# Kernel tuning notes

Hardware: AMD Instinct MI355X
Metric: run time of the kernel (lower is better)

The kernel has to match this reference:

```python
import jax, jax.numpy as jnp
import numpy as np
import math

B, S, D = 4, 2048, 1024

def setup_inputs() -> dict:
    key = jax.random.key(0)
    k1, k2, k3, k4 = jax.random.split(key, 4)
    scale = 1.0 / math.sqrt(D)
    return {
        "x": jax.random.normal(k1, (B, S, D), dtype=jnp.float32),
        "w_q": jax.random.normal(k2, (D, D), dtype=jnp.float32) * scale,
        "w_k": jax.random.normal(k3, (D, D), dtype=jnp.float32) * scale,
        "w_v": jax.random.normal(k4, (D, D), dtype=jnp.float32) * scale,
        "causal": 1,
    }

def reference(x, w_q, w_k, w_v, causal):
    # QKV projections: nn.Linear(dim, dim, bias=False) -> x @ W.T
    q = jnp.einsum('bsd,ed->bse', x, w_q)
    k = jnp.einsum('bsd,ed->bse', x, w_k)
    v = jnp.einsum('bsd,ed->bse', x, w_v)
    d_k = q.shape[-1]
    scores = jnp.einsum('bqd,bkd->bqk', q, k) / jnp.sqrt(jnp.asarray(d_k, q.dtype))
    if causal:
        seq_len = q.shape[-2]
        mask = jnp.triu(jnp.ones((seq_len, seq_len), dtype=bool), k=1)
        scores = jnp.where(mask, jnp.asarray(-jnp.inf, scores.dtype), scores)
    weights = jax.nn.softmax(scores, axis=-1)
    return jnp.einsum('bqk,bkd->bqd', weights, v)
```

## Files before the change

### kernel.cpp

```cpp
#include <hip/hip_runtime.h>
#include <stdint.h>

typedef unsigned short u16;
typedef __attribute__((ext_vector_type(8))) __bf16 bf16x8;
typedef __attribute__((ext_vector_type(4))) float f32x4;

__device__ __forceinline__ u16 f2bf(float f) {
  unsigned u = __float_as_uint(f);
  u += 0x7FFF + ((u >> 16) & 1);
  return (u16)(u >> 16);
}

__device__ __forceinline__ float bf2f(u16 h) {
  return __uint_as_float(((unsigned)h) << 16);
}

__device__ __forceinline__ void llds16(const u16* g, u16* l) {
  __builtin_amdgcn_global_load_lds(
      (const __attribute__((address_space(1))) void*)g,
      (__attribute__((address_space(3))) void*)l, 16, 0, 0);
}

__global__ __launch_bounds__(256) void cast_all(
    const float* __restrict__ x, const float* __restrict__ wq,
    const float* __restrict__ wk, const float* __restrict__ wv,
    u16* __restrict__ xb, u16* __restrict__ wb, float* __restrict__ lsum) {
  int i = blockIdx.x * 256 + threadIdx.x;
  if (i < 8192) lsum[i] = 0.f;
  const float* src; u16* dst; int off;
  if (i < 2097152)      { src = x;  dst = xb;            off = i; }
  else if (i < 2359296) { src = wq; dst = wb;            off = i - 2097152; }
  else if (i < 2621440) { src = wk; dst = wb + 1048576;  off = i - 2359296; }
  else                  { src = wv; dst = wb + 2097152;  off = i - 2621440; }
  float4 f = ((const float4*)src)[off];
  ushort4 o;
  o.x = f2bf(f.x); o.y = f2bf(f.y); o.z = f2bf(f.z); o.w = f2bf(f.w);
  ((ushort4*)dst)[off] = o;
}

template<int MODE>
__global__ __launch_bounds__(256) void gemm_nt(
    const u16* __restrict__ A, long long sA, int lda,
    const u16* __restrict__ B, long long sB, int ldb,
    void* __restrict__ Cp, long long sC, int ldc,
    int K, u16* __restrict__ vt, float scale,
    float* __restrict__ lsum, const int* __restrict__ causalp) {
  const int t = threadIdx.x;
  const int causal = (MODE == 0) ? 1 : causalp[0];

  int rt = blockIdx.x, ct = blockIdx.y;

  const int rowbase = rt * 128;
  const int colbase = ct * 128;
  const u16* Ab = A + (long long)blockIdx.z * sA;
  const u16* Bb = B + (long long)blockIdx.z * sB;

  int Keff = K;
  if (MODE == 2 && causal) Keff = min(K, rowbase + 128);

  __shared__ u16 As[8192];
  __shared__ u16 Bs[8192];

  const int lane = t & 63;
  const int wv = t >> 6;
  const int wr = wv >> 1;
  const int wc = wv & 1;
  const int quad = lane >> 4;
  const int lr = lane & 15;

  f32x4 acc[4][4];
  const f32x4 zero = {0.f, 0.f, 0.f, 0.f};
#pragma unroll
  for (int i = 0; i < 4; ++i)
#pragma unroll
    for (int j = 0; j < 4; ++j) acc[i][j] = zero;

  {
    const int csw = (t & 7) ^ ((t >> 3) & 7);
    const u16* ga = Ab + (long long)(rowbase + (t >> 3)) * lda + csw * 8;
    const u16* gb = Bb + (long long)(colbase + (t >> 3)) * ldb + csw * 8;
    const long long ra = 32LL * lda, rb = 32LL * ldb;
    u16* la = As + t * 8;
    u16* lb = Bs + t * 8;

    const int m7 = lr & 7;
    const int a_base = (wr * 64 + lr) * 64 + ((quad ^ m7) * 8);
    const int b_base = (wc * 64 + lr) * 64 + ((quad ^ m7) * 8);

    for (int k0 = 0; k0 < Keff; k0 += 64) {
      __syncthreads();
#pragma unroll
      for (int i = 0; i < 4; ++i) {
        llds16(ga + k0 + i * ra, la + i * 2048);
        llds16(gb + k0 + i * rb, lb + i * 2048);
      }
      __syncthreads();
#pragma unroll
      for (int ks = 0; ks < 2; ++ks) {
        const int ko = ks ? 32 : 0;
        bf16x8 af[4], bfv[4];
#pragma unroll
        for (int tm = 0; tm < 4; ++tm)
          af[tm] = *(const bf16x8*)(As + ((a_base + tm * 1024) ^ ko));
#pragma unroll
        for (int tn = 0; tn < 4; ++tn)
          bfv[tn] = *(const bf16x8*)(Bs + ((b_base + tn * 1024) ^ ko));
#pragma unroll
        for (int tm = 0; tm < 4; ++tm)
#pragma unroll
          for (int tn = 0; tn < 4; ++tn)
            acc[tm][tn] = __builtin_amdgcn_mfma_f32_16x16x32_bf16(
                af[tm], bfv[tn], acc[tm][tn], 0, 0, 0);
      }
    }
  }

  if (MODE == 0 && colbase >= 2048) {
#pragma unroll
    for (int tm = 0; tm < 4; ++tm) {
      int s0 = rowbase + wr * 64 + tm * 16 + quad * 4;
      int b = s0 >> 11;
      int sl = s0 & 2047;
#pragma unroll
      for (int tn = 0; tn < 4; ++tn) {
        int e = colbase - 2048 + wc * 64 + tn * 16 + lr;
        ushort4 o;
        o.x = f2bf(acc[tm][tn][0]);
        o.y = f2bf(acc[tm][tn][1]);
        o.z = f2bf(acc[tm][tn][2]);
        o.w = f2bf(acc[tm][tn][3]);
        *(ushort4*)(vt + ((long long)(b * 1024 + e)) * 2048 + sl) = o;
      }
    }
    return;
  }

#pragma unroll
  for (int tm = 0; tm < 4; ++tm) {
#pragma unroll
    for (int r = 0; r < 4; ++r) {
      const int grow = rowbase + wr * 64 + tm * 16 + quad * 4 + r;
      float li, rsum = 0.f;
      if (MODE == 2) li = __builtin_amdgcn_rcpf(lsum[blockIdx.z * 2048 + grow]);
#pragma unroll
      for (int tn = 0; tn < 4; ++tn) {
        const int gcol = colbase + wc * 64 + tn * 16 + lr;
        float val = acc[tm][tn][r];
        if (MODE == 0) {
          ((u16*)Cp)[(long long)grow * ldc + gcol] = f2bf(val);
        } else if (MODE == 1) {
          u16* C = (u16*)Cp + (long long)blockIdx.z * sC;
          float ex = (causal && gcol > grow) ? 0.f : __expf(val * scale);
          C[(long long)grow * ldc + gcol] = f2bf(ex);
          rsum += ex;
        } else {
          float* C = (float*)Cp + (long long)blockIdx.z * sC;
          C[(long long)grow * ldc + gcol] = val * li;
        }
      }
      if (MODE == 1) {
#pragma unroll
        for (int o = 8; o > 0; o >>= 1) rsum += __shfl_xor(rsum, o, 64);
        if (lr == 0)
          atomicAdd(&lsum[blockIdx.z * 2048 + grow], rsum);
      }
    }
  }
}

template<int MODE>
__device__ __forceinline__ void gemm_core(
    int rt, int ct, int zb, int causal, u16* As, u16* Bs,
    const u16* __restrict__ A, long long sA, int lda,
    const u16* __restrict__ B, long long sB, int ldb,
    void* __restrict__ Cp, long long sC, int ldc,
    int K, float scale, float* __restrict__ lsum) {
  const int t = threadIdx.x;

  const int rowbase = rt * 128;
  const int colbase = ct * 128;
  const u16* Ab = A + (long long)zb * sA;
  const u16* Bb = B + (long long)zb * sB;

  int Keff = K;
  if (MODE == 2 && causal) Keff = min(K, rowbase + 128);

  const int lane = t & 63;
  const int wv = t >> 6;
  const int wr = wv >> 1;
  const int wc = wv & 1;
  const int quad = lane >> 4;
  const int lr = lane & 15;

  f32x4 acc[4][4];
  const f32x4 zero = {0.f, 0.f, 0.f, 0.f};
#pragma unroll
  for (int i = 0; i < 4; ++i)
#pragma unroll
    for (int j = 0; j < 4; ++j) acc[i][j] = zero;

  {
    const int csw = (t & 7) ^ ((t >> 3) & 7);
    const u16* ga = Ab + (long long)(rowbase + (t >> 3)) * lda + csw * 8;
    const u16* gb = Bb + (long long)(colbase + (t >> 3)) * ldb + csw * 8;
    const long long ra = 32LL * lda, rb = 32LL * ldb;
    u16* la = As + t * 8;
    u16* lb = Bs + t * 8;

    const int m7 = lr & 7;
    const int a_base = (wr * 64 + lr) * 64 + ((quad ^ m7) * 8);
    const int b_base = (wc * 64 + lr) * 64 + ((quad ^ m7) * 8);

#pragma unroll
    for (int i = 0; i < 4; ++i) {
      llds16(ga + i * ra, la + i * 2048);
      llds16(gb + i * rb, lb + i * 2048);
    }
    __syncthreads();
    for (int k0 = 0; k0 < Keff; k0 += 64) {
      const int nb = ((k0 >> 6) & 1) ^ 1;
      const int bo = (nb ^ 1) << 13;
      if (k0 + 64 < Keff) {
#pragma unroll
        for (int i = 0; i < 4; ++i) {
          llds16(ga + (k0 + 64) + i * ra, la + nb * 8192 + i * 2048);
          llds16(gb + (k0 + 64) + i * rb, lb + nb * 8192 + i * 2048);
        }
      }
#pragma unroll
      for (int ks = 0; ks < 2; ++ks) {
        const int ko = ks ? 32 : 0;
        bf16x8 af[4], bfv[4];
#pragma unroll
        for (int tm = 0; tm < 4; ++tm)
          af[tm] = *(const bf16x8*)(As + bo + ((a_base + tm * 1024) ^ ko));
#pragma unroll
        for (int tn = 0; tn < 4; ++tn)
          bfv[tn] = *(const bf16x8*)(Bs + bo + ((b_base + tn * 1024) ^ ko));
#pragma unroll
        for (int tm = 0; tm < 4; ++tm)
#pragma unroll
          for (int tn = 0; tn < 4; ++tn)
            acc[tm][tn] = __builtin_amdgcn_mfma_f32_16x16x32_bf16(
                af[tm], bfv[tn], acc[tm][tn], 0, 0, 0);
      }
      __syncthreads();
    }
  }

#pragma unroll
  for (int tm = 0; tm < 4; ++tm) {
#pragma unroll
    for (int r = 0; r < 4; ++r) {
      const int grow = rowbase + wr * 64 + tm * 16 + quad * 4 + r;
      float li, rsum = 0.f;
      if (MODE == 2) li = __builtin_amdgcn_rcpf(lsum[zb * 2048 + grow]);
#pragma unroll
      for (int tn = 0; tn < 4; ++tn) {
        const int gcol = colbase + wc * 64 + tn * 16 + lr;
        float val = acc[tm][tn][r];
        if (MODE == 1) {
          u16* C = (u16*)Cp + (long long)zb * sC;
          float ex = (causal && gcol > grow) ? 0.f : __expf(val * scale);
          C[(long long)grow * ldc + gcol] = f2bf(ex);
          rsum += ex;
        } else {
          float* C = (float*)Cp + (long long)zb * sC;
          C[(long long)grow * ldc + gcol] = val * li;
        }
      }
      if (MODE == 1) {
#pragma unroll
        for (int o = 8; o > 0; o >>= 1) rsum += __shfl_xor(rsum, o, 64);
        if (lr == 0)
          atomicAdd(&lsum[zb * 2048 + grow], rsum);
      }
    }
  }
}

__global__ __launch_bounds__(256) void gemm_sc(
    const u16* __restrict__ qk, u16* __restrict__ sb,
    float* __restrict__ lsum, const int* __restrict__ causalp) {
  __shared__ u16 As[16384];
  __shared__ u16 Bs[16384];
  const int causal = causalp[0];
  const int zb = blockIdx.z;
  const int xcd = blockIdx.x & 7;
  const int chunk = ((blockIdx.x >> 3) + 8 * blockIdx.z) & 31;
  int rt, ct;
  if (chunk < 17) {
    int i2 = xcd * 17 + chunk, c = 0;
    while (i2 >= 16 - c) { i2 -= 16 - c; ++c; }
    ct = c; rt = c + i2;
  } else {
    if (causal) return;
    int i2 = xcd * 15 + (chunk - 17), r = 0;
    while (i2 >= r + 1) { i2 -= r + 1; ++r; }
    rt = i2; ct = r + 1;
  }
  gemm_core<1>(rt, ct, zb, causal, As, Bs,
               qk, 2048LL * 2048, 2048, qk + 1024, 2048LL * 2048, 2048,
               sb, 2048LL * 2048, 2048, 1024, 0.03125f, lsum);
}

__global__ __launch_bounds__(256) void gemm_pv(
    const u16* __restrict__ sb, const u16* __restrict__ vtb,
    float* __restrict__ out, float* __restrict__ lsum,
    const int* __restrict__ causalp) {
  __shared__ u16 As[16384];
  __shared__ u16 Bs[16384];
  const int causal = causalp[0];
  const int s = ((blockIdx.x & 7) << 6) + (blockIdx.x >> 3);
  const int zb = s >> 7;
  const int ct = (s & 127) >> 4;
  const int m = s & 15;
  const int rt = (s & 32) ? m : 15 - m;
  gemm_core<2>(rt, ct, zb, causal, As, Bs,
               sb, 2048LL * 2048, 2048, vtb, 1024LL * 2048, 2048,
               out, 2048LL * 1024, 1024, 2048, 1.0f, lsum);
}

extern "C" void kernel_launch(void* const* d_in, const int* in_sizes, int n_in,
                              void* d_out, int out_size, void* d_ws, size_t ws_size,
                              hipStream_t stream) {
  const float* x  = (const float*)d_in[0];
  const float* wq = (const float*)d_in[1];
  const float* wk = (const float*)d_in[2];
  const float* wv = (const float*)d_in[3];
  const int* causal = (const int*)d_in[4];
  float* out = (float*)d_out;

  char* ws = (char*)d_ws;
  u16* xb = (u16*)(ws);
  u16* wb = (u16*)(ws + 16777216);
  u16* qk = (u16*)(ws + 23068672);
  u16* vt = (u16*)(ws + 56623104);
  u16* sb = (u16*)(ws + 73400320);
  float* lsum = (float*)(ws + 106954752);

  cast_all<<<11264, 256, 0, stream>>>(x, wq, wk, wv, xb, wb, lsum);

  gemm_nt<0><<<dim3(64, 24, 1), 256, 0, stream>>>(
      xb, 0, 1024, wb, 0, 1024, qk, 0, 2048, 1024, vt, 1.0f, nullptr, causal);

  gemm_sc<<<dim3(256, 1, 4), 256, 0, stream>>>(qk, sb, lsum, causal);

  gemm_pv<<<dim3(512, 1, 1), 256, 0, stream>>>(sb, vt, out, lsum, causal);
}
```

Baseline: 231.3 us.

## Replace 128x128 four-wave attention GEMMs with single-wave 64x64 tile kernels

The score and PV GEMMs move from 256-thread blocks computing 128x128 tiles with double-buffered LDS to 64-thread single-wave blocks computing 64x64 tiles with one LDS buffer. The aim is finer causal skipping, since only lower-triangle 64x64 tiles run and the PV K range is trimmed per 64 rows, plus more blocks to fill the CUs. In exchange, each tile reuses its loaded data less, global-to-LDS prefetch overlap is gone because every K step syncs around a fresh load, and the XCD-aware block ordering is dropped.

```diff
diff --git a/kernel.cpp b/kernel.cpp
--- a/kernel.cpp
+++ b/kernel.cpp
@@ -169,74 +169,81 @@
 }
 
 template<int MODE>
-__device__ __forceinline__ void gemm_core(
-    int rt, int ct, int zb, int causal, u16* As, u16* Bs,
+__global__ __launch_bounds__(64) void tile64(
     const u16* __restrict__ A, long long sA, int lda,
     const u16* __restrict__ B, long long sB, int ldb,
     void* __restrict__ Cp, long long sC, int ldc,
-    int K, float scale, float* __restrict__ lsum) {
+    int K, float scale, float* __restrict__ lsum,
+    const int* __restrict__ causalp) {
   const int t = threadIdx.x;
-
-  const int rowbase = rt * 128;
-  const int colbase = ct * 128;
+  const int causal = causalp[0];
+
+  int rt, ct, zb;
+  if (MODE == 1) {
+    const int j = blockIdx.x;
+    zb = j >> 10;
+    const int rem = j & 1023;
+    rt = rem >> 5;
+    ct = rem & 31;
+    if (causal && ct > rt) return;
+  } else {
+    const int j = blockIdx.x;
+    zb = j >> 9;
+    const int rem = j & 511;
+    rt = 31 - (rem >> 4);
+    ct = rem & 15;
+  }
+
+  const int rowbase = rt * 64;
+  const int colbase = ct * 64;
   const u16* Ab = A + (long long)zb * sA;
   const u16* Bb = B + (long long)zb * sB;
 
   int Keff = K;
-  if (MODE == 2 && causal) Keff = min(K, rowbase + 128);
-
-  const int lane = t & 63;
-  const int wv = t >> 6;
-  const int wr = wv >> 1;
-  const int wc = wv & 1;
-  const int quad = lane >> 4;
-  const int lr = lane & 15;
+  if (MODE == 2 && causal) Keff = min(K, rowbase + 64);
+
+  __shared__ u16 As[4096];
+  __shared__ u16 Bs[4096];
+
+  const int quad = t >> 4;
+  const int lr = t & 15;
 
   f32x4 acc[4][4];
   const f32x4 zero = {0.f, 0.f, 0.f, 0.f};
 #pragma unroll
   for (int i = 0; i < 4; ++i)
 #pragma unroll
-    for (int j = 0; j < 4; ++j) acc[i][j] = zero;
+    for (int j2 = 0; j2 < 4; ++j2) acc[i][j2] = zero;
 
   {
     const int csw = (t & 7) ^ ((t >> 3) & 7);
     const u16* ga = Ab + (long long)(rowbase + (t >> 3)) * lda + csw * 8;
     const u16* gb = Bb + (long long)(colbase + (t >> 3)) * ldb + csw * 8;
-    const long long ra = 32LL * lda, rb = 32LL * ldb;
+    const long long ra = 8LL * lda, rb = 8LL * ldb;
     u16* la = As + t * 8;
     u16* lb = Bs + t * 8;
 
     const int m7 = lr & 7;
-    const int a_base = (wr * 64 + lr) * 64 + ((quad ^ m7) * 8);
-    const int b_base = (wc * 64 + lr) * 64 + ((quad ^ m7) * 8);
-
-#pragma unroll
-    for (int i = 0; i < 4; ++i) {
-      llds16(ga + i * ra, la + i * 2048);
-      llds16(gb + i * rb, lb + i * 2048);
-    }
-    __syncthreads();
+    const int fbase = lr * 64 + ((quad ^ m7) * 8);
+
     for (int k0 = 0; k0 < Keff; k0 += 64) {
-      const int nb = ((k0 >> 6) & 1) ^ 1;
-      const int bo = (nb ^ 1) << 13;
-      if (k0 + 64 < Keff) {
-#pragma unroll
-        for (int i = 0; i < 4; ++i) {
-          llds16(ga + (k0 + 64) + i * ra, la + nb * 8192 + i * 2048);
-          llds16(gb + (k0 + 64) + i * rb, lb + nb * 8192 + i * 2048);
-        }
-      }
+      __syncthreads();
+#pragma unroll
+      for (int i = 0; i < 8; ++i) {
+        llds16(ga + k0 + i * ra, la + i * 512);
+        llds16(gb + k0 + i * rb, lb + i * 512);
+      }
+      __syncthreads();
 #pragma unroll
       for (int ks = 0; ks < 2; ++ks) {
         const int ko = ks ? 32 : 0;
         bf16x8 af[4], bfv[4];
 #pragma unroll
         for (int tm = 0; tm < 4; ++tm)
-          af[tm] = *(const bf16x8*)(As + bo + ((a_base + tm * 1024) ^ ko));
+          af[tm] = *(const bf16x8*)(As + ((fbase + tm * 1024) ^ ko));
 #pragma unroll
         for (int tn = 0; tn < 4; ++tn)
-          bfv[tn] = *(const bf16x8*)(Bs + bo + ((b_base + tn * 1024) ^ ko));
+          bfv[tn] = *(const bf16x8*)(Bs + ((fbase + tn * 1024) ^ ko));
 #pragma unroll
         for (int tm = 0; tm < 4; ++tm)
 #pragma unroll
@@ -244,7 +251,6 @@
             acc[tm][tn] = __builtin_amdgcn_mfma_f32_16x16x32_bf16(
                 af[tm], bfv[tn], acc[tm][tn], 0, 0, 0);
       }
-      __syncthreads();
     }
   }
 
@@ -252,12 +258,12 @@
   for (int tm = 0; tm < 4; ++tm) {
 #pragma unroll
     for (int r = 0; r < 4; ++r) {
-      const int grow = rowbase + wr * 64 + tm * 16 + quad * 4 + r;
+      const int grow = rowbase + tm * 16 + quad * 4 + r;
       float li, rsum = 0.f;
       if (MODE == 2) li = __builtin_amdgcn_rcpf(lsum[zb * 2048 + grow]);
 #pragma unroll
       for (int tn = 0; tn < 4; ++tn) {
-        const int gcol = colbase + wc * 64 + tn * 16 + lr;
+        const int gcol = colbase + tn * 16 + lr;
         float val = acc[tm][tn][r];
         if (MODE == 1) {
           u16* C = (u16*)Cp + (long long)zb * sC;
@@ -279,48 +285,6 @@
   }
 }
 
-__global__ __launch_bounds__(256) void gemm_sc(
-    const u16* __restrict__ qk, u16* __restrict__ sb,
-    float* __restrict__ lsum, const int* __restrict__ causalp) {
-  __shared__ u16 As[16384];
-  __shared__ u16 Bs[16384];
-  const int causal = causalp[0];
-  const int zb = blockIdx.z;
-  const int xcd = blockIdx.x & 7;
-  const int chunk = ((blockIdx.x >> 3) + 8 * blockIdx.z) & 31;
-  int rt, ct;
-  if (chunk < 17) {
-    int i2 = xcd * 17 + chunk, c = 0;
-    while (i2 >= 16 - c) { i2 -= 16 - c; ++c; }
-    ct = c; rt = c + i2;
-  } else {
-    if (causal) return;
-    int i2 = xcd * 15 + (chunk - 17), r = 0;
-    while (i2 >= r + 1) { i2 -= r + 1; ++r; }
-    rt = i2; ct = r + 1;
-  }
-  gemm_core<1>(rt, ct, zb, causal, As, Bs,
-               qk, 2048LL * 2048, 2048, qk + 1024, 2048LL * 2048, 2048,
-               sb, 2048LL * 2048, 2048, 1024, 0.03125f, lsum);
-}
-
-__global__ __launch_bounds__(256) void gemm_pv(
-    const u16* __restrict__ sb, const u16* __restrict__ vtb,
-    float* __restrict__ out, float* __restrict__ lsum,
-    const int* __restrict__ causalp) {
-  __shared__ u16 As[16384];
-  __shared__ u16 Bs[16384];
-  const int causal = causalp[0];
-  const int s = ((blockIdx.x & 7) << 6) + (blockIdx.x >> 3);
-  const int zb = s >> 7;
-  const int ct = (s & 127) >> 4;
-  const int m = s & 15;
-  const int rt = (s & 32) ? m : 15 - m;
-  gemm_core<2>(rt, ct, zb, causal, As, Bs,
-               sb, 2048LL * 2048, 2048, vtb, 1024LL * 2048, 2048,
-               out, 2048LL * 1024, 1024, 2048, 1.0f, lsum);
-}
-
 extern "C" void kernel_launch(void* const* d_in, const int* in_sizes, int n_in,
                               void* d_out, int out_size, void* d_ws, size_t ws_size,
                               hipStream_t stream) {
@@ -344,7 +308,11 @@
   gemm_nt<0><<<dim3(64, 24, 1), 256, 0, stream>>>(
       xb, 0, 1024, wb, 0, 1024, qk, 0, 2048, 1024, vt, 1.0f, nullptr, causal);
 
-  gemm_sc<<<dim3(256, 1, 4), 256, 0, stream>>>(qk, sb, lsum, causal);
-
-  gemm_pv<<<dim3(512, 1, 1), 256, 0, stream>>>(sb, vt, out, lsum, causal);
-}
+  tile64<1><<<dim3(4096, 1, 1), 64, 0, stream>>>(
+      qk, 2048LL * 2048, 2048, qk + 1024, 2048LL * 2048, 2048,
+      sb, 2048LL * 2048, 2048, 1024, 0.03125f, lsum, causal);
+
+  tile64<2><<<dim3(2048, 1, 1), 64, 0, stream>>>(
+      sb, 2048LL * 2048, 2048, vt, 1024LL * 2048, 2048,
+      out, 2048LL * 1024, 1024, 2048, 1.0f, lsum, causal);
+}
```

Result: slower. 252.4 us (+9.1%).
